# Optimization experiments

Measured on AMD Instinct MI355X. Metric: run time of the kernel, lower is better.

## Reference

```python
import jax, jax.numpy as jnp
import numpy as np

D_MODEL = 1024
N_HEADS = 16
D_HEAD = D_MODEL // N_HEADS


def setup_inputs() -> dict:
    key = jax.random.key(0)
    k1, k2, k3 = jax.random.split(key, 3)
    x = jax.random.normal(k1, (2, 2048, D_MODEL), dtype=jnp.float32)
    # Dense layer params (glorot-ish scale)
    W_qkv = jax.random.normal(k2, (D_MODEL, 3 * D_MODEL), dtype=jnp.float32) * (1.0 / np.sqrt(D_MODEL))
    b_qkv = jnp.zeros((3 * D_MODEL,), dtype=jnp.float32)
    W_proj = jax.random.normal(k3, (D_MODEL, D_MODEL), dtype=jnp.float32) * (1.0 / np.sqrt(D_MODEL))
    b_proj = jnp.zeros((D_MODEL,), dtype=jnp.float32)
    return {"x": x, "W_qkv": W_qkv, "b_qkv": b_qkv, "W_proj": W_proj, "b_proj": b_proj}


def reference(x, W_qkv, b_qkv, W_proj, b_proj):
    B, S, _ = x.shape
    qkv = x @ W_qkv + b_qkv                      # [B,S,3D]
    q, k, v = jnp.split(qkv, 3, axis=-1)
    # [B,S,D] -> [B,H,S,Dh]
    def to_heads(t):
        return t.reshape(B, S, N_HEADS, D_HEAD).transpose(0, 2, 1, 3)
    q, k, v = to_heads(q), to_heads(k), to_heads(v)
    scores = jnp.einsum('bhqd,bhkd->bhqk', q, k)  # [B,H,S,S]
    causal = jnp.tril(jnp.ones((S, S), dtype=bool))
    # NOTE: mask applied BEFORE scaling, matching the original module.
    scores = jnp.where(causal[None, None, :, :], scores, jnp.float32(-1e9))
    scaled = scores / jnp.sqrt(jnp.float32(D_HEAD))
    attn = jax.nn.softmax(scaled, axis=-1)
    ctx = jnp.einsum('bhqk,bhkd->bhqd', attn, v)  # [B,H,S,Dh]
    ctx = ctx.transpose(0, 2, 1, 3).reshape(B, S, D_MODEL)
    return ctx @ W_proj + b_proj
```

## Files before the change

kernel.cpp:

```cpp
#include <hip/hip_runtime.h>
#include <stdint.h>

typedef __attribute__((ext_vector_type(8))) short short8;
typedef __attribute__((ext_vector_type(4))) float f32x4;

#define QSCALE 0.18033688011112043f

__device__ __forceinline__ unsigned short f2b(float f) {
  union { float f; uint32_t u; } v; v.f = f;
  uint32_t u = v.u;
  u = u + 0x7fffu + ((u >> 16) & 1u);
  return (unsigned short)(u >> 16);
}
__device__ __forceinline__ unsigned int cvtpk(float lo, float hi) {
  unsigned int r;
  asm("v_cvt_pk_bf16_f32 %0, %1, %2" : "=v"(r) : "v"(lo), "v"(hi));
  return r;
}
__device__ __forceinline__ void gload16(const void* g, void* lds) {
  __builtin_amdgcn_global_load_lds((const __attribute__((address_space(1))) void*)g,
                                   (__attribute__((address_space(3))) void*)lds, 16, 0, 0);
}

__global__ __launch_bounds__(256) void cvt_f32_bf16(const float* __restrict__ in,
                                                    unsigned short* __restrict__ out, int n) {
  int i = (blockIdx.x * 256 + threadIdx.x) * 4;
  if (i < n) {
    float4 v = *(const float4*)(in + i);
    ushort4 o;
    o.x = f2b(v.x); o.y = f2b(v.y); o.z = f2b(v.z); o.w = f2b(v.w);
    *(ushort4*)(out + i) = o;
  }
}

__global__ __launch_bounds__(256) void transposeW(const float* __restrict__ W,
                                                  unsigned short* __restrict__ Wt,
                                                  int K, int N, float scale, int scaleRows) {
  __shared__ float tile[32][33];
  int x0 = blockIdx.x * 32, y0 = blockIdx.y * 32;
  int tx = threadIdx.x, ty = threadIdx.y;
  #pragma unroll
  for (int j = 0; j < 4; ++j)
    tile[ty + j * 8][tx] = W[(size_t)(y0 + ty + j * 8) * N + x0 + tx];
  __syncthreads();
  #pragma unroll
  for (int j = 0; j < 4; ++j) {
    int orow = x0 + ty + j * 8;
    float s = (orow < scaleRows) ? scale : 1.0f;
    Wt[(size_t)orow * K + y0 + tx] = f2b(tile[tx][ty + j * 8] * s);
  }
}

template<bool OUTF32, int BN>
__global__ __launch_bounds__(256, 3) void gemm_bt(const unsigned short* __restrict__ A,
                                                  const unsigned short* __restrict__ Bt,
                                                  const float* __restrict__ bias,
                                                  void* __restrict__ outp,
                                                  unsigned short* __restrict__ vtOut,
                                                  int M, int N, int K,
                                                  float bscale, int bscaleN, int mtiles) {
  constexpr int FN = BN / 32;
  __shared__ unsigned short As[2][128 * 64];
  __shared__ unsigned short Bs[2][BN * 64];
  const int t = threadIdx.x;
  const int lane = t & 63;
  const int w = t >> 6;
  const int wm = w >> 1, wn = w & 1;

  const int cpx = gridDim.x >> 3;
  const int swz = (blockIdx.x & 7) * cpx + (blockIdx.x >> 3);
  const int m0 = (swz % mtiles) * 128;
  const int n0 = (swz / mtiles) * BN;

  const f32x4 zero = {0.f, 0.f, 0.f, 0.f};
  f32x4 acc[4][FN];
  #pragma unroll
  for (int i = 0; i < 4; ++i)
    #pragma unroll
    for (int j = 0; j < FN; ++j) acc[i][j] = zero;

  const int cl = lane & 15, g = lane >> 4;
  const int srow = t >> 3;
  const int sch  = (t & 7) ^ (srow & 7);

  auto stage = [&](int k0, int buf) {
    #pragma unroll
    for (int r = 0; r < 4; ++r)
      gload16(A + (size_t)(m0 + r * 32 + srow) * K + k0 + sch * 8,
              (char*)As[buf] + r * 4096 + t * 16);
    #pragma unroll
    for (int r = 0; r < BN / 32; ++r)
      gload16(Bt + (size_t)(n0 + r * 32 + srow) * K + k0 + sch * 8,
              (char*)Bs[buf] + r * 4096 + t * 16);
  };

  stage(0, 0);
  __syncthreads();

  const int nk = K >> 6;
  for (int ki = 0; ki < nk; ++ki) {
    const int cur = ki & 1;
    if (ki + 1 < nk) stage((ki + 1) << 6, cur ^ 1);
    char* AsB = (char*)As[cur];
    char* BsB = (char*)Bs[cur];
    #pragma unroll
    for (int kk = 0; kk < 2; ++kk) {
      short8 af[4], bfr[FN];
      #pragma unroll
      for (int f = 0; f < 4; ++f) {
        int arow = wm * 64 + f * 16 + cl;
        af[f]  = *(const short8*)(AsB + ((arow * 128 + kk * 64 + g * 16) ^ ((cl & 7) << 4)));
      }
      #pragma unroll
      for (int f = 0; f < FN; ++f) {
        int brow = wn * (BN / 2) + f * 16 + cl;
        bfr[f] = *(const short8*)(BsB + ((brow * 128 + kk * 64 + g * 16) ^ ((cl & 7) << 4)));
      }
      #pragma unroll
      for (int fm = 0; fm < 4; ++fm)
        #pragma unroll
        for (int fn = 0; fn < FN; ++fn)
          acc[fm][fn] = __builtin_amdgcn_mfma_f32_16x16x32_bf16(af[fm], bfr[fn], acc[fm][fn], 0, 0, 0);
    }
    __syncthreads();
  }

  const bool vpath = (!OUTF32) && (vtOut != nullptr) && (n0 >= 2048);
  #pragma unroll
  for (int fn = 0; fn < FN; ++fn) {
    int col = n0 + wn * (BN / 2) + fn * 16 + cl;
    float bv = bias[col] * ((col < bscaleN) ? bscale : 1.0f);
    if (vpath) {
      int hcol = col - 2048;
      size_t vrow = (size_t)hcol * 2048;
      #pragma unroll
      for (int fm = 0; fm < 4; ++fm) {
        int rbase = m0 + wm * 64 + fm * 16 + g * 4;
        int b = rbase >> 11, s = rbase & 2047;
        ushort4 ov;
        ov.x = f2b(acc[fm][fn][0] + bv);
        ov.y = f2b(acc[fm][fn][1] + bv);
        ov.z = f2b(acc[fm][fn][2] + bv);
        ov.w = f2b(acc[fm][fn][3] + bv);
        *(ushort4*)(vtOut + (size_t)b * 1024 * 2048 + vrow + s) = ov;
      }
    } else {
      #pragma unroll
      for (int fm = 0; fm < 4; ++fm) {
        int rbase = m0 + wm * 64 + fm * 16 + g * 4;
        #pragma unroll
        for (int r = 0; r < 4; ++r) {
          float vout = acc[fm][fn][r] + bv;
          if (OUTF32) ((float*)outp)[(size_t)(rbase + r) * N + col] = vout;
          else ((unsigned short*)outp)[(size_t)(rbase + r) * N + col] = f2b(vout);
        }
      }
    }
  }
}

__global__ __launch_bounds__(256, 3) void attn_mfma3(const unsigned short* __restrict__ qkv,
                                                     const unsigned short* __restrict__ Vt,
                                                     unsigned short* __restrict__ ctx) {
  const int idx = blockIdx.x;
  const int bh = ((idx & 7) << 2) | ((idx >> 3) & 3);
  const int qt = 31 - (idx >> 5);
  const int b = bh >> 4, h = bh & 15;
  const int t = threadIdx.x;
  const int l = t & 63;
  const int w = t >> 6;
  const int cl = l & 15;
  const int g  = l >> 4;

  __shared__ unsigned short Ks[2][64 * 64];
  __shared__ unsigned short Vs[2][64 * 64];
  __shared__ unsigned short Ps[4][16 * 64];
  __shared__ unsigned short Ones[16 * 64];

  char* Pbuf = (char*)(&Ps[w][0]);
  char* OnB = (char*)Ones;

  const size_t kbase  = (size_t)(b * 2048) * 3072 + 1024 + h * 64;
  const size_t vtbase = (size_t)(bh * 64) * 2048;

  auto stage = [&](int jt, int buf) {
    #pragma unroll
    for (int i = 0; i < 2; ++i) {
      int row = i * 32 + w * 8 + (l >> 3);
      int ch  = (l & 7) ^ (l >> 3);
      gload16(qkv + kbase + (size_t)(jt * 64 + row) * 3072 + ch * 8,
              (char*)Ks[buf] + i * 4096 + w * 1024);
      gload16(Vt + vtbase + (size_t)row * 2048 + jt * 64 + ch * 8,
              (char*)Vs[buf] + i * 4096 + w * 1024);
    }
  };

  {
    int row = t >> 4;
    int c4  = (t & 15) * 4;
    unsigned short vv = (row == 0) ? (unsigned short)0x3F80 : (unsigned short)0;
    ushort4 ov = {vv, vv, vv, vv};
    *(ushort4*)(OnB + ((row * 128 + c4 * 2) ^ ((row & 7) << 4))) = ov;
  }

  stage(0, 0);
  __syncthreads();

  short8 a5[2];
  #pragma unroll
  for (int kk = 0; kk < 2; ++kk)
    a5[kk] = *(const short8*)(OnB + ((cl * 128 + kk * 64 + g * 16) ^ ((cl & 7) << 4)));

  short8 bq[2];
  {
    const unsigned short* qp = qkv + (size_t)(b * 2048 + qt * 64 + w * 16 + cl) * 3072 + h * 64 + g * 8;
    bq[0] = *(const short8*)(qp);
    bq[1] = *(const short8*)(qp + 32);
  }

  f32x4 o[4], o5;
  #pragma unroll
  for (int c = 0; c < 4; ++c) o[c] = (f32x4){0.f, 0.f, 0.f, 0.f};
  o5 = (f32x4){0.f, 0.f, 0.f, 0.f};
  float m = -1e30f;

  for (int jt = 0; jt <= qt; ++jt) {
    const int cur = jt & 1;
    if (jt < qt) stage(jt + 1, cur ^ 1);
    char* KsB = (char*)Ks[cur];
    char* VsB = (char*)Vs[cur];

    short8 ak[4][2];
    #pragma unroll
    for (int tt = 0; tt < 4; ++tt)
      #pragma unroll
      for (int kk = 0; kk < 2; ++kk)
        ak[tt][kk] = *(const short8*)(KsB + (((tt * 16 + cl) * 128 + kk * 64 + g * 16) ^ ((cl & 7) << 4)));
    short8 av[4][2];
    #pragma unroll
    for (int c = 0; c < 4; ++c)
      #pragma unroll
      for (int kk = 0; kk < 2; ++kk)
        av[c][kk] = *(const short8*)(VsB + (((c * 16 + cl) * 128 + kk * 64 + g * 16) ^ ((cl & 7) << 4)));

    f32x4 st[4];
    #pragma unroll
    for (int tt = 0; tt < 4; ++tt) st[tt] = (f32x4){0.f, 0.f, 0.f, 0.f};
    __builtin_amdgcn_s_setprio(1);
    #pragma unroll
    for (int kk = 0; kk < 2; ++kk)
      #pragma unroll
      for (int tt = 0; tt < 4; ++tt)
        st[tt] = __builtin_amdgcn_mfma_f32_16x16x32_bf16(ak[tt][kk], bq[kk], st[tt], 0, 0, 0);
    __builtin_amdgcn_s_setprio(0);

    float z[4][4];
    #pragma unroll
    for (int tt = 0; tt < 4; ++tt)
      #pragma unroll
      for (int r = 0; r < 4; ++r) z[tt][r] = st[tt][r];
    if (jt == qt) {
      int q_loc = w * 16 + cl;
      #pragma unroll
      for (int tt = 0; tt < 4; ++tt)
        #pragma unroll
        for (int r = 0; r < 4; ++r)
          if (tt * 16 + 4 * g + r > q_loc) z[tt][r] = -1e30f;
    }
    float m0a = fmaxf(fmaxf(z[0][0], z[0][1]), fmaxf(z[0][2], z[0][3]));
    float m1a = fmaxf(fmaxf(z[1][0], z[1][1]), fmaxf(z[1][2], z[1][3]));
    float m2a = fmaxf(fmaxf(z[2][0], z[2][1]), fmaxf(z[2][2], z[2][3]));
    float m3a = fmaxf(fmaxf(z[3][0], z[3][1]), fmaxf(z[3][2], z[3][3]));
    float cm = fmaxf(fmaxf(m0a, m1a), fmaxf(m2a, m3a));
    cm = fmaxf(cm, __shfl_xor(cm, 16));
    cm = fmaxf(cm, __shfl_xor(cm, 32));

    if (!__all(cm <= m + 8.f)) {
      float mn = fmaxf(m, cm);
      float alpha = exp2f(m - mn);
      m = mn;
      #pragma unroll
      for (int c = 0; c < 4; ++c)
        #pragma unroll
        for (int r = 0; r < 4; ++r) o[c][r] *= alpha;
      o5[0] *= alpha;
    }

    #pragma unroll
    for (int tt = 0; tt < 4; ++tt) {
      float p0 = exp2f(z[tt][0] - m), p1 = exp2f(z[tt][1] - m);
      float p2 = exp2f(z[tt][2] - m), p3 = exp2f(z[tt][3] - m);
      uint2 val;
      val.x = cvtpk(p0, p1);
      val.y = cvtpk(p2, p3);
      *(uint2*)(Pbuf + ((cl * 128 + tt * 32 + g * 8) ^ ((cl & 7) << 4))) = val;
    }
    short8 bp[2];
    #pragma unroll
    for (int kk = 0; kk < 2; ++kk)
      bp[kk] = *(const short8*)(Pbuf + ((cl * 128 + kk * 64 + g * 16) ^ ((cl & 7) << 4)));

    __builtin_amdgcn_s_setprio(1);
    #pragma unroll
    for (int kk = 0; kk < 2; ++kk) {
      #pragma unroll
      for (int c = 0; c < 4; ++c)
        o[c] = __builtin_amdgcn_mfma_f32_16x16x32_bf16(av[c][kk], bp[kk], o[c], 0, 0, 0);
      o5 = __builtin_amdgcn_mfma_f32_16x16x32_bf16(a5[kk], bp[kk], o5, 0, 0, 0);
    }
    __builtin_amdgcn_s_setprio(0);

    __syncthreads();
  }

  float lsum = __shfl(o5[0], cl);
  float inv = 1.f / lsum;
  unsigned short* crow = ctx + (size_t)(b * 2048 + qt * 64 + w * 16 + cl) * 1024 + h * 64 + g * 4;
  #pragma unroll
  for (int c = 0; c < 4; ++c) {
    uint2 val;
    val.x = cvtpk(o[c][0] * inv, o[c][1] * inv);
    val.y = cvtpk(o[c][2] * inv, o[c][3] * inv);
    *(uint2*)(crow + c * 16) = val;
  }
}

extern "C" void kernel_launch(void* const* d_in, const int* in_sizes, int n_in,
                              void* d_out, int out_size, void* d_ws, size_t ws_size,
                              hipStream_t stream) {
  const float* x     = (const float*)d_in[0];
  const float* Wqkv  = (const float*)d_in[1];
  const float* bqkv  = (const float*)d_in[2];
  const float* Wproj = (const float*)d_in[3];
  const float* bproj = (const float*)d_in[4];
  float* out = (float*)d_out;

  char* ws = (char*)d_ws;
  unsigned short* xb     = (unsigned short*)(ws);
  unsigned short* wqkvT  = (unsigned short*)(ws + 8388608);
  unsigned short* wprojT = (unsigned short*)(ws + 14680064);
  unsigned short* qkv    = (unsigned short*)(ws + 16777216);
  unsigned short* ctx    = (unsigned short*)(ws + 41943040);
  unsigned short* vt     = (unsigned short*)(ws + 50331648);

  cvt_f32_bf16<<<4096, 256, 0, stream>>>(x, xb, 4096 * 1024);

  dim3 tb(32, 8);
  transposeW<<<dim3(3072 / 32, 1024 / 32), tb, 0, stream>>>(Wqkv, wqkvT, 1024, 3072, QSCALE, 1024);
  transposeW<<<dim3(1024 / 32, 1024 / 32), tb, 0, stream>>>(Wproj, wprojT, 1024, 1024, 1.0f, 0);

  gemm_bt<false, 128><<<768, 256, 0, stream>>>(xb, wqkvT, bqkv, qkv, vt,
                                               4096, 3072, 1024, QSCALE, 1024, 32);

  attn_mfma3<<<1024, 256, 0, stream>>>(qkv, vt, ctx);

  gemm_bt<true, 64><<<512, 256, 0, stream>>>(ctx, wprojT, bproj, out, nullptr,
                                             4096, 1024, 1024, 1.0f, 0, 32);
}
```

Before: 191.8 us.

## Halve GEMM K-step to 32 and pack two row halves per LDS row

The bf16 GEMM now stages K in steps of 32 instead of 64. Each 128-byte LDS row holds the 32-wide K slices of two rows (row r and row r+64, or r+BH for B), with an XOR swizzle. This halves LDS use per block, which could allow more resident blocks and reduce LDS pressure. In exchange there are twice as many main-loop iterations and barriers, and less MFMA work between syncs.

```diff
diff --git a/kernel.cpp b/kernel.cpp
--- a/kernel.cpp
+++ b/kernel.cpp
@@ -60,8 +60,9 @@
                                                   int M, int N, int K,
                                                   float bscale, int bscaleN, int mtiles) {
   constexpr int FN = BN / 32;
-  __shared__ unsigned short As[2][128 * 64];
-  __shared__ unsigned short Bs[2][BN * 64];
+  constexpr int BH = BN / 2;
+  __shared__ unsigned short As[2][64 * 64];
+  __shared__ unsigned short Bs[2][BH * 64];
   const int t = threadIdx.x;
   const int lane = t & 63;
   const int w = t >> 6;
@@ -80,55 +81,57 @@
     for (int j = 0; j < FN; ++j) acc[i][j] = zero;
 
   const int cl = lane & 15, g = lane >> 4;
-  const int srow = t >> 3;
-  const int sch  = (t & 7) ^ (srow & 7);
+  const int prow = t >> 3;
+  const int pc   = (t & 7) ^ (prow & 7);
 
   auto stage = [&](int k0, int buf) {
     #pragma unroll
-    for (int r = 0; r < 4; ++r)
-      gload16(A + (size_t)(m0 + r * 32 + srow) * K + k0 + sch * 8,
+    for (int r = 0; r < 2; ++r) {
+      int lrow = r * 32 + prow + 64 * (pc >> 2);
+      gload16(A + (size_t)(m0 + lrow) * K + k0 + (pc & 3) * 8,
               (char*)As[buf] + r * 4096 + t * 16);
-    #pragma unroll
-    for (int r = 0; r < BN / 32; ++r)
-      gload16(Bt + (size_t)(n0 + r * 32 + srow) * K + k0 + sch * 8,
+    }
+    #pragma unroll
+    for (int r = 0; r < BN / 64; ++r) {
+      int lrow = r * 32 + prow + BH * (pc >> 2);
+      gload16(Bt + (size_t)(n0 + lrow) * K + k0 + (pc & 3) * 8,
               (char*)Bs[buf] + r * 4096 + t * 16);
+    }
   };
 
   stage(0, 0);
   __syncthreads();
 
-  const int nk = K >> 6;
+  const int nk = K >> 5;
   for (int ki = 0; ki < nk; ++ki) {
     const int cur = ki & 1;
-    if (ki + 1 < nk) stage((ki + 1) << 6, cur ^ 1);
+    if (ki + 1 < nk) stage((ki + 1) << 5, cur ^ 1);
     char* AsB = (char*)As[cur];
     char* BsB = (char*)Bs[cur];
-    #pragma unroll
-    for (int kk = 0; kk < 2; ++kk) {
-      short8 af[4], bfr[FN];
-      #pragma unroll
-      for (int f = 0; f < 4; ++f) {
-        int arow = wm * 64 + f * 16 + cl;
-        af[f]  = *(const short8*)(AsB + ((arow * 128 + kk * 64 + g * 16) ^ ((cl & 7) << 4)));
-      }
-      #pragma unroll
-      for (int f = 0; f < FN; ++f) {
-        int brow = wn * (BN / 2) + f * 16 + cl;
-        bfr[f] = *(const short8*)(BsB + ((brow * 128 + kk * 64 + g * 16) ^ ((cl & 7) << 4)));
-      }
-      #pragma unroll
-      for (int fm = 0; fm < 4; ++fm)
-        #pragma unroll
-        for (int fn = 0; fn < FN; ++fn)
-          acc[fm][fn] = __builtin_amdgcn_mfma_f32_16x16x32_bf16(af[fm], bfr[fn], acc[fm][fn], 0, 0, 0);
-    }
+    short8 af[4], bfr[FN];
+    #pragma unroll
+    for (int f = 0; f < 4; ++f) {
+      int pr = f * 16 + cl;
+      af[f] = *(const short8*)(AsB + pr * 128 + ((((wm << 2) + g) ^ (pr & 7)) << 4));
+    }
+    #pragma unroll
+    for (int f = 0; f < FN; ++f) {
+      int lr = wn * BH + f * 16 + cl;
+      int pr = lr & (BH - 1);
+      bfr[f] = *(const short8*)(BsB + pr * 128 + ((((wn << 2) + g) ^ (pr & 7)) << 4));
+    }
+    #pragma unroll
+    for (int fm = 0; fm < 4; ++fm)
+      #pragma unroll
+      for (int fn = 0; fn < FN; ++fn)
+        acc[fm][fn] = __builtin_amdgcn_mfma_f32_16x16x32_bf16(af[fm], bfr[fn], acc[fm][fn], 0, 0, 0);
     __syncthreads();
   }
 
   const bool vpath = (!OUTF32) && (vtOut != nullptr) && (n0 >= 2048);
   #pragma unroll
   for (int fn = 0; fn < FN; ++fn) {
-    int col = n0 + wn * (BN / 2) + fn * 16 + cl;
+    int col = n0 + wn * BH + fn * 16 + cl;
     float bv = bias[col] * ((col < bscaleN) ? bscale : 1.0f);
     if (vpath) {
       int hcol = col - 2048;
```

Result: faster. 181.5 us (-5.4%).
